# Kernel tuning notes

Measured on AMD Instinct MI355X. Metric: run time of the kernel, lower is better.

The kernel has to match this reference:

```python
import jax, jax.numpy as jnp
import numpy as np

NC = 6          # num_classes
RM = 16         # reg_max
TOPK = 10       # tal_topk
IMG = 640.0
STRIDES = (8, 16, 32)
BS = 32
NGT = 20        # GT boxes per image (uniform -> static max_boxes)


def _iou(b1, b2, ciou, eps=1e-7):
    x1 = jnp.maximum(b1[..., 0], b2[..., 0]); y1 = jnp.maximum(b1[..., 1], b2[..., 1])
    x2 = jnp.minimum(b1[..., 2], b2[..., 2]); y2 = jnp.minimum(b1[..., 3], b2[..., 3])
    inter = jnp.maximum(x2 - x1, 0.0) * jnp.maximum(y2 - y1, 0.0)
    w1 = jnp.maximum(b1[..., 2] - b1[..., 0], eps); h1 = jnp.maximum(b1[..., 3] - b1[..., 1], eps)
    w2 = jnp.maximum(b2[..., 2] - b2[..., 0], eps); h2 = jnp.maximum(b2[..., 3] - b2[..., 1], eps)
    union = w1 * h1 + w2 * h2 - inter + eps
    iou = inter / union
    if not ciou:
        return iou
    cw = jnp.maximum(b1[..., 2], b2[..., 2]) - jnp.minimum(b1[..., 0], b2[..., 0])
    ch = jnp.maximum(b1[..., 3], b2[..., 3]) - jnp.minimum(b1[..., 1], b2[..., 1])
    c2 = cw ** 2 + ch ** 2 + eps
    rho2 = ((b1[..., 0] + b1[..., 2] - b2[..., 0] - b2[..., 2]) ** 2
            + (b1[..., 1] + b1[..., 3] - b2[..., 1] - b2[..., 3]) ** 2) / 4.0
    v = (4.0 / (np.pi ** 2)) * (jnp.arctan(w2 / h2) - jnp.arctan(w1 / h1)) ** 2
    alpha = jax.lax.stop_gradient(v / (v - iou + (1.0 + eps)))
    return iou - (rho2 / c2 + v * alpha)


def _forward(p0, p1, p2, targets):
    bs = p0.shape[0]
    regs, clss, ancs, strs = [], [], [], []
    for p, s in zip((p0, p1, p2), STRIDES):
        b, c, h, w = p.shape
        p = jnp.transpose(p, (0, 2, 3, 1)).reshape(b, h * w, c)
        regs.append(p[..., :4 * RM].reshape(b, h * w, 4, RM))
        clss.append(p[..., 4 * RM:])
        gy, gx = jnp.meshgrid(jnp.arange(h), jnp.arange(w), indexing='ij')
        ancs.append(((jnp.stack([gx, gy], -1).astype(jnp.float32) + 0.5) * s).reshape(-1, 2))
        strs.append(jnp.full((h * w, 1), float(s), jnp.float32))
    pred_reg = jnp.concatenate(regs, 1)      # [bs, A, 4, RM]
    pred_cls = jnp.concatenate(clss, 1)      # [bs, A, NC]
    anchors = jnp.concatenate(ancs, 0)       # [A, 2] pixel coords
    stride_a = jnp.concatenate(strs, 0)      # [A, 1]
    A = anchors.shape[0]

    proj = jnp.arange(RM, dtype=jnp.float32)
    pd_dist = jnp.sum(jax.nn.softmax(pred_reg, -1) * proj, -1)       # [bs, A, 4]
    anc_b = jnp.broadcast_to(anchors[None], (bs, A, 2))
    pd_boxes = jnp.concatenate([anc_b - pd_dist[..., :2] * stride_a,
                                anc_b + pd_dist[..., 2:] * stride_a], -1)

    # GT parse: exactly NGT rows per image, grouped by image index (static reshape)
    G = targets.shape[0] // bs
    t = targets.reshape(bs, G, 6)
    gt_labels = t[..., 1]
    xywh = t[..., 2:6] * IMG
    gt_boxes = jnp.concatenate([xywh[..., :2] - xywh[..., 2:] / 2,
                                xywh[..., :2] + xywh[..., 2:] / 2], -1)  # [bs, G, 4]
    mask_gt = jnp.ones((bs, G, 1), jnp.float32)

    # ---- task-aligned assignment (on detached preds) ----
    pscore = jax.nn.sigmoid(jax.lax.stop_gradient(pred_cls))
    pbox_d = jax.lax.stop_gradient(pd_boxes)
    ious = _iou(gt_boxes[:, :, None, :], pbox_d[:, None, :, :], False)   # [bs, G, A]
    labels_i = gt_labels.astype(jnp.int32)
    scores = jnp.einsum('bac,bgc->bga', pscore, jax.nn.one_hot(labels_i, NC, dtype=pscore.dtype))
    align = (scores ** 0.5) * (ious ** 6.0)
    lt = anc_b[:, None, :, :] - gt_boxes[:, :, None, :2]
    rb = gt_boxes[:, :, None, 2:] - anc_b[:, None, :, :]
    in_gts = jnp.min(jnp.concatenate([lt, rb], -1), -1) > 1e-9
    align = align * in_gts * mask_gt
    _, tk_idx = jax.lax.top_k(align, TOPK)
    bi = jnp.arange(bs)[:, None, None]; gi = jnp.arange(G)[None, :, None]
    mask_pos = jnp.zeros((bs, G, A), bool).at[bi, gi, tk_idx].set(True)
    mask_pos = mask_pos & (align > 0)
    multi = jnp.sum(mask_pos, 1) > 1                                   # [bs, A]
    full = jnp.moveaxis(jax.nn.one_hot(jnp.argmax(align, 1), G), -1, 1) > 0.5
    mask_pos = jnp.where(multi[:, None, :], full, mask_pos)

    fg = jnp.any(mask_pos, 1)                                          # [bs, A]
    gt_idx = jnp.argmax(mask_pos, 1)                                   # [bs, A] (first True)
    tb = jnp.take_along_axis(gt_boxes, jnp.broadcast_to(gt_idx[..., None], (bs, A, 4)), axis=1)
    target_boxes = jnp.where(fg[..., None], tb, 0.0)
    t_lab = jnp.take_along_axis(labels_i, gt_idx, axis=1)
    iou_fg = jnp.maximum(jax.lax.stop_gradient(_iou(pd_boxes, target_boxes, False)), 0.0)
    norm_align = align / (jnp.max(align, -1, keepdims=True) + 1e-9)
    norm_g = jnp.take_along_axis(norm_align, gt_idx[:, None, :], axis=1)[:, 0, :]
    sval = jnp.where(fg, norm_g * iou_fg, 0.0)
    target_scores = sval[..., None] * jax.nn.one_hot(t_lab, NC, dtype=jnp.float32)

    # cls: BCE with logits, sum / num_anchors
    x = pred_cls
    bce = jnp.maximum(x, 0.0) - x * target_scores + jnp.log1p(jnp.exp(-jnp.abs(x)))
    loss_cls = jnp.sum(bce) / float(A)

    fgf = fg.astype(jnp.float32)
    num_pos = jnp.maximum(jnp.sum(fgf), 1.0)

    # bbox: 1 - CIoU over positives
    ciou = _iou(pd_boxes, target_boxes, True)
    loss_bbox = jnp.sum((1.0 - ciou) * fgf) / num_pos

    # DFL
    ltrb = jnp.concatenate([(anc_b - target_boxes[..., :2]) / stride_a,
                            (target_boxes[..., 2:] - anc_b) / stride_a], -1)
    ltrb = jnp.clip(ltrb, 0.0, RM - 1.01)
    tl = ltrb.astype(jnp.int32)
    wl = (tl + 1).astype(jnp.float32) - ltrb
    wr = ltrb - tl.astype(jnp.float32)
    logZ = jax.nn.logsumexp(pred_reg, -1)                              # [bs, A, 4]
    ce_l = logZ - jnp.take_along_axis(pred_reg, tl[..., None], -1)[..., 0]
    ce_r = logZ - jnp.take_along_axis(pred_reg, (tl + 1)[..., None], -1)[..., 0]
    loss_dfl = jnp.sum(jnp.sum(ce_l * wl + ce_r * wr, -1) * fgf) / num_pos

    l_cls = loss_cls * 1.0
    l_bbox = loss_bbox * 7.5
    l_dfl = loss_dfl * 1.5
    return jnp.stack([l_cls + l_bbox + l_dfl, l_cls, l_bbox, jnp.asarray(0.0, jnp.float32), l_dfl])


def setup_inputs() -> dict:
    key = jax.random.key(0)
    k0, k1, k2, k3, k4, k5 = jax.random.split(key, 6)
    C = 4 * RM + NC
    p0 = jax.random.normal(k0, (BS, C, 80, 80), jnp.float32)
    p1 = jax.random.normal(k1, (BS, C, 40, 40), jnp.float32)
    p2 = jax.random.normal(k2, (BS, C, 20, 20), jnp.float32)
    bidx = jnp.repeat(jnp.arange(BS), NGT).astype(jnp.float32)
    lab = jax.random.randint(k3, (BS * NGT,), 0, NC).astype(jnp.float32)
    cxcy = jax.random.uniform(k4, (BS * NGT, 2), minval=0.2, maxval=0.8)
    wh = jax.random.uniform(k5, (BS * NGT, 2), minval=0.05, maxval=0.3)
    targets = jnp.concatenate([bidx[:, None], lab[:, None], cxcy, wh], 1)
    return {"p0": p0, "p1": p1, "p2": p2, "targets": targets}


def reference(p0, p1, p2, targets):
    return _forward(p0, p1, p2, targets)
```

## Files before the change

kernel.cpp:

```cpp
#include <hip/hip_runtime.h>
#include <math.h>

#define NC 6
#define RM 16
#define TOPK 10
#define BSZ 32
#define G 20
#define A_TOT 8400
#define NBA (BSZ * A_TOT)
#define NBLK_LOSS ((NBA + 255) / 256)
#define MAXCAND 1024

__device__ __forceinline__ void anchor_decode(int a, int& lvl, int& ai, int& w, int& hw, float& s) {
    if (a < 6400)      { lvl = 0; ai = a;        w = 80; hw = 6400; s = 8.f; }
    else if (a < 8000) { lvl = 1; ai = a - 6400; w = 40; hw = 1600; s = 16.f; }
    else               { lvl = 2; ai = a - 8000; w = 20; hw = 400;  s = 32.f; }
}

__global__ __launch_bounds__(256) void k_prep(
        const float* __restrict__ p0, const float* __restrict__ p1, const float* __restrict__ p2,
        float* __restrict__ pd_boxes, float* __restrict__ logZ, float* __restrict__ pcls) {
    int idx = blockIdx.x * 256 + threadIdx.x;
    if (idx >= NBA) return;
    int b = idx / A_TOT, a = idx % A_TOT;
    int lvl, ai, w, hw; float s;
    anchor_decode(a, lvl, ai, w, hw, s);
    const float* p = (lvl == 0) ? p0 : ((lvl == 1) ? p1 : p2);
    const float* base = p + (size_t)b * 70 * hw + ai;
    float ax = ((ai % w) + 0.5f) * s;
    float ay = ((ai / w) + 0.5f) * s;

    float dist[4], lz[4];
    for (int sd = 0; sd < 4; ++sd) {
        float v[RM];
        float m = -1e30f;
        #pragma unroll
        for (int k = 0; k < RM; ++k) {
            v[k] = base[(size_t)(sd * RM + k) * hw];
            m = fmaxf(m, v[k]);
        }
        float se = 0.f, sk = 0.f;
        #pragma unroll
        for (int k = 0; k < RM; ++k) {
            float e = expf(v[k] - m);
            se += e;
            sk += e * (float)k;
        }
        dist[sd] = sk / se;
        lz[sd] = m + logf(se);
    }
    float4 box;
    box.x = ax - dist[0] * s;
    box.y = ay - dist[1] * s;
    box.z = ax + dist[2] * s;
    box.w = ay + dist[3] * s;
    ((float4*)pd_boxes)[idx] = box;
    ((float4*)logZ)[idx] = make_float4(lz[0], lz[1], lz[2], lz[3]);
    #pragma unroll
    for (int c = 0; c < NC; ++c)
        pcls[(size_t)c * NBA + idx] = base[(size_t)(64 + c) * hw];
}

__device__ __forceinline__ bool cand_better(float av, int ai_, float bv, int bi_) {
    if (av > bv) return true;
    if (av < bv) return false;
    if (ai_ < 0) return false;
    if (bi_ < 0) return true;
    return ai_ < bi_;
}

__global__ __launch_bounds__(256) void k_align(
        const float* __restrict__ targets,
        const float* __restrict__ pd_boxes, const float* __restrict__ pcls,
        float* __restrict__ align, float* __restrict__ amax, unsigned int* __restrict__ mask) {
    __shared__ float cval[MAXCAND];
    __shared__ int   cidx[MAXCAND];
    __shared__ int   cnt_s;
    __shared__ float rv[4];
    __shared__ int   ri[4];
    __shared__ float win_v_s;
    __shared__ int   win_i_s;

    int bg = blockIdx.x;
    int b = bg / G;
    int g = bg % G;
    const float* t = targets + (size_t)bg * 6;
    float cx = t[2] * 640.f, cy = t[3] * 640.f;
    float hw_ = t[4] * 320.f, hh = t[5] * 320.f;
    float gx1 = cx - hw_, gy1 = cy - hh, gx2 = cx + hw_, gy2 = cy + hh;
    int lab = (int)t[1];
    const float* pc = pcls + (size_t)lab * NBA + (size_t)b * A_TOT;
    const float4* pb = (const float4*)pd_boxes + (size_t)b * A_TOT;
    float* arow = align + (size_t)bg * A_TOT;
    const float eps = 1e-7f;
    float gw = fmaxf(gx2 - gx1, eps), gh = fmaxf(gy2 - gy1, eps);
    float garea = gw * gh;

    if (threadIdx.x == 0) cnt_s = 0;
    __syncthreads();

    for (int a = threadIdx.x; a < A_TOT; a += 256) {
        float4 box = pb[a];
        float x1 = fmaxf(gx1, box.x), y1 = fmaxf(gy1, box.y);
        float x2 = fminf(gx2, box.z), y2 = fminf(gy2, box.w);
        float inter = fmaxf(x2 - x1, 0.f) * fmaxf(y2 - y1, 0.f);
        float w2 = fmaxf(box.z - box.x, eps), h2 = fmaxf(box.w - box.y, eps);
        float uni = garea + w2 * h2 - inter + eps;
        float iou = inter / uni;
        float sc = 1.f / (1.f + expf(-pc[a]));
        int lvl, ai, w_, hwc; float s;
        anchor_decode(a, lvl, ai, w_, hwc, s);
        float ax = ((ai % w_) + 0.5f) * s, ay = ((ai / w_) + 0.5f) * s;
        float mn = fminf(fminf(ax - gx1, ay - gy1), fminf(gx2 - ax, gy2 - ay));
        float al = 0.f;
        if (mn > 1e-9f) {
            float i2 = iou * iou;
            al = sqrtf(sc) * (i2 * i2 * i2);
        }
        arow[a] = al;
        if (al > 0.f) {
            int p = atomicAdd(&cnt_s, 1);
            if (p < MAXCAND) { cval[p] = al; cidx[p] = a; }
        }
    }
    __syncthreads();
    int cnt = min(cnt_s, MAXCAND);

    float mv[MAXCAND / 256];
    int   mi[MAXCAND / 256];
    #pragma unroll
    for (int r = 0; r < MAXCAND / 256; ++r) {
        int p = threadIdx.x + r * 256;
        mv[r] = (p < cnt) ? cval[p] : -1.f;
        mi[r] = (p < cnt) ? cidx[p] : -1;
    }

    int lane = threadIdx.x & 63, wv = threadIdx.x >> 6;
    for (int it = 0; it < TOPK; ++it) {
        float v = -1.f; int vi = -1;
        #pragma unroll
        for (int r = 0; r < MAXCAND / 256; ++r)
            if (cand_better(mv[r], mi[r], v, vi)) { v = mv[r]; vi = mi[r]; }
        #pragma unroll
        for (int off = 32; off > 0; off >>= 1) {
            float ov = __shfl_down(v, off);
            int   oi = __shfl_down(vi, off);
            if (cand_better(ov, oi, v, vi)) { v = ov; vi = oi; }
        }
        if (lane == 0) { rv[wv] = v; ri[wv] = vi; }
        __syncthreads();
        if (threadIdx.x == 0) {
            float v0 = rv[0]; int i0 = ri[0];
            for (int i = 1; i < 4; ++i)
                if (cand_better(rv[i], ri[i], v0, i0)) { v0 = rv[i]; i0 = ri[i]; }
            if (it == 0) amax[bg] = fmaxf(v0, 0.f);
            if (i0 >= 0 && v0 > 0.f) atomicOr(&mask[(size_t)b * A_TOT + i0], 1u << g);
            win_v_s = v0; win_i_s = i0;
        }
        __syncthreads();
        int wi = win_i_s;
        if (wi < 0) break;
        #pragma unroll
        for (int r = 0; r < MAXCAND / 256; ++r)
            if (mi[r] == wi) { mv[r] = -1.f; mi[r] = -1; }
    }
}

__global__ __launch_bounds__(256) void k_loss(
        const float* __restrict__ targets,
        const float* __restrict__ pd_boxes, const float* __restrict__ logZ,
        const float* __restrict__ pcls, const float* __restrict__ align,
        const float* __restrict__ amax, const unsigned int* __restrict__ mask,
        const float* __restrict__ p0, const float* __restrict__ p1, const float* __restrict__ p2,
        float* __restrict__ partial) {
    int idx = blockIdx.x * 256 + threadIdx.x;
    float bce_s = 0.f, bbox_s = 0.f, dfl_s = 0.f, fg_s = 0.f;
    if (idx < NBA) {
        int b = idx / A_TOT, a = idx % A_TOT;
        unsigned int m = mask[idx];
        if (__popc(m) > 1) {
            float best = -1.f; int bg_ = 0;
            for (int g = 0; g < G; ++g) {
                float x = align[((size_t)b * G + g) * A_TOT + a];
                if (x > best) { best = x; bg_ = g; }
            }
            m = 1u << bg_;
        }
        bool fg = (m != 0u);
        float4 box = ((const float4*)pd_boxes)[idx];
        float tbx1 = 0.f, tby1 = 0.f, tbx2 = 0.f, tby2 = 0.f;
        float sval = 0.f; int lab = -1;
        const float eps = 1e-7f;
        if (fg) {
            int gidx = __ffs(m) - 1;
            const float* t = targets + ((size_t)b * G + gidx) * 6;
            lab = (int)t[1];
            float cx = t[2] * 640.f, cy = t[3] * 640.f;
            float hw_ = t[4] * 320.f, hh = t[5] * 320.f;
            tbx1 = cx - hw_; tby1 = cy - hh; tbx2 = cx + hw_; tby2 = cy + hh;
            float x1 = fmaxf(box.x, tbx1), y1 = fmaxf(box.y, tby1);
            float x2 = fminf(box.z, tbx2), y2 = fminf(box.w, tby2);
            float inter = fmaxf(x2 - x1, 0.f) * fmaxf(y2 - y1, 0.f);
            float w1 = fmaxf(box.z - box.x, eps), h1 = fmaxf(box.w - box.y, eps);
            float w2 = fmaxf(tbx2 - tbx1, eps), h2 = fmaxf(tby2 - tby1, eps);
            float uni = w1 * h1 + w2 * h2 - inter + eps;
            float iou_fg = fmaxf(inter / uni, 0.f);
            float al = align[((size_t)b * G + gidx) * A_TOT + a];
            sval = (al / (amax[b * G + gidx] + 1e-9f)) * iou_fg;
            fg_s = 1.f;
        }
        #pragma unroll
        for (int c = 0; c < NC; ++c) {
            float x = pcls[(size_t)c * NBA + idx];
            float ts = (fg && c == lab) ? sval : 0.f;
            bce_s += fmaxf(x, 0.f) - x * ts + log1pf(expf(-fabsf(x)));
        }
        if (fg) {
            float x1 = fmaxf(box.x, tbx1), y1 = fmaxf(box.y, tby1);
            float x2 = fminf(box.z, tbx2), y2 = fminf(box.w, tby2);
            float inter = fmaxf(x2 - x1, 0.f) * fmaxf(y2 - y1, 0.f);
            float w1 = fmaxf(box.z - box.x, eps), h1 = fmaxf(box.w - box.y, eps);
            float w2 = fmaxf(tbx2 - tbx1, eps), h2 = fmaxf(tby2 - tby1, eps);
            float uni = w1 * h1 + w2 * h2 - inter + eps;
            float iou = inter / uni;
            float cw = fmaxf(box.z, tbx2) - fminf(box.x, tbx1);
            float ch = fmaxf(box.w, tby2) - fminf(box.y, tby1);
            float c2 = cw * cw + ch * ch + eps;
            float dx = box.x + box.z - tbx1 - tbx2;
            float dy = box.y + box.w - tby1 - tby2;
            float rho2 = (dx * dx + dy * dy) * 0.25f;
            float dv = atanf(w2 / h2) - atanf(w1 / h1);
            float v = 0.40528473f * dv * dv;
            float alpha = v / (v - iou + (1.f + eps));
            float ciou = iou - (rho2 / c2 + v * alpha);
            bbox_s = 1.f - ciou;
            int lvl, ai, w_, hwc; float s;
            anchor_decode(a, lvl, ai, w_, hwc, s);
            float ax = ((ai % w_) + 0.5f) * s, ay = ((ai / w_) + 0.5f) * s;
            const float* p = (lvl == 0) ? p0 : ((lvl == 1) ? p1 : p2);
            const float* base = p + (size_t)b * 70 * hwc + ai;
            float4 lzv = ((const float4*)logZ)[idx];
            float lz[4] = {lzv.x, lzv.y, lzv.z, lzv.w};
            float lt[4] = {(ax - tbx1) / s, (ay - tby1) / s, (tbx2 - ax) / s, (tby2 - ay) / s};
            #pragma unroll
            for (int sd = 0; sd < 4; ++sd) {
                float d = fminf(fmaxf(lt[sd], 0.f), (float)RM - 1.01f);
                int tl = (int)d;
                float wl = (float)(tl + 1) - d;
                float wr = d - (float)tl;
                float xl = base[(size_t)(sd * RM + tl) * hwc];
                float xr = base[(size_t)(sd * RM + tl + 1) * hwc];
                dfl_s += (lz[sd] - xl) * wl + (lz[sd] - xr) * wr;
            }
        }
    }
    __shared__ float part[4][4];
    int lane = threadIdx.x & 63, wv = threadIdx.x >> 6;
    #pragma unroll
    for (int off = 32; off > 0; off >>= 1) {
        bce_s  += __shfl_down(bce_s,  off);
        bbox_s += __shfl_down(bbox_s, off);
        dfl_s  += __shfl_down(dfl_s,  off);
        fg_s   += __shfl_down(fg_s,   off);
    }
    if (lane == 0) {
        part[wv][0] = bce_s; part[wv][1] = bbox_s;
        part[wv][2] = dfl_s; part[wv][3] = fg_s;
    }
    __syncthreads();
    if (threadIdx.x == 0) {
        float s0 = 0.f, s1 = 0.f, s2 = 0.f, s3 = 0.f;
        for (int i = 0; i < 4; ++i) {
            s0 += part[i][0]; s1 += part[i][1]; s2 += part[i][2]; s3 += part[i][3];
        }
        float4* pp = (float4*)partial;
        pp[blockIdx.x] = make_float4(s0, s1, s2, s3);
    }
}

__global__ __launch_bounds__(256) void k_final(const float* __restrict__ partial,
                                               float* __restrict__ out) {
    double s0 = 0., s1 = 0., s2 = 0., s3 = 0.;
    for (int i = threadIdx.x; i < NBLK_LOSS; i += 256) {
        float4 p = ((const float4*)partial)[i];
        s0 += p.x; s1 += p.y; s2 += p.z; s3 += p.w;
    }
    #pragma unroll
    for (int off = 32; off > 0; off >>= 1) {
        s0 += __shfl_down(s0, off);
        s1 += __shfl_down(s1, off);
        s2 += __shfl_down(s2, off);
        s3 += __shfl_down(s3, off);
    }
    __shared__ double part[4][4];
    int lane = threadIdx.x & 63, wv = threadIdx.x >> 6;
    if (lane == 0) { part[wv][0] = s0; part[wv][1] = s1; part[wv][2] = s2; part[wv][3] = s3; }
    __syncthreads();
    if (threadIdx.x == 0) {
        double bce = 0., bbox = 0., dfl = 0., fgc = 0.;
        for (int i = 0; i < 4; ++i) {
            bce += part[i][0]; bbox += part[i][1]; dfl += part[i][2]; fgc += part[i][3];
        }
        double l_cls = bce / (double)A_TOT;
        double np_ = fmax(fgc, 1.0);
        double l_bbox = 7.5 * bbox / np_;
        double l_dfl = 1.5 * dfl / np_;
        out[0] = (float)(l_cls + l_bbox + l_dfl);
        out[1] = (float)l_cls;
        out[2] = (float)l_bbox;
        out[3] = 0.f;
        out[4] = (float)l_dfl;
    }
}

extern "C" void kernel_launch(void* const* d_in, const int* in_sizes, int n_in,
                              void* d_out, int out_size, void* d_ws, size_t ws_size,
                              hipStream_t stream) {
    const float* p0 = (const float*)d_in[0];
    const float* p1 = (const float*)d_in[1];
    const float* p2 = (const float*)d_in[2];
    const float* targets = (const float*)d_in[3];
    float* out = (float*)d_out;

    char* ws = (char*)d_ws;
    size_t off = 0;
    float* pd_boxes = (float*)(ws + off); off += (size_t)NBA * 4 * sizeof(float);
    float* logZ     = (float*)(ws + off); off += (size_t)NBA * 4 * sizeof(float);
    float* pcls     = (float*)(ws + off); off += (size_t)NC * NBA * sizeof(float);
    float* align    = (float*)(ws + off); off += (size_t)BSZ * G * A_TOT * sizeof(float);
    float* amax     = (float*)(ws + off); off += (size_t)BSZ * G * sizeof(float);
    unsigned int* mask = (unsigned int*)(ws + off); off += (size_t)NBA * sizeof(unsigned int);
    float* partial  = (float*)(ws + off); off += (size_t)NBLK_LOSS * 4 * sizeof(float);

    hipMemsetAsync(mask, 0, (size_t)NBA * sizeof(unsigned int), stream);

    k_prep<<<(NBA + 255) / 256, 256, 0, stream>>>(p0, p1, p2, pd_boxes, logZ, pcls);
    k_align<<<BSZ * G, 256, 0, stream>>>(targets, pd_boxes, pcls, align, amax, mask);
    k_loss<<<NBLK_LOSS, 256, 0, stream>>>(targets, pd_boxes, logZ, pcls, align,
                                          amax, mask, p0, p1, p2, partial);
    k_final<<<1, 256, 0, stream>>>(partial, out);
}
```

Baseline: 151.6 us.

## Vectorize prep, recompute align scores instead of storing them, split BCE

```diff
diff --git a/kernel.cpp b/kernel.cpp
--- a/kernel.cpp
+++ b/kernel.cpp
@@ -9,7 +9,10 @@
 #define A_TOT 8400
 #define NBA (BSZ * A_TOT)
 #define NBLK_LOSS ((NBA + 255) / 256)
+#define NBLK_PREP ((NBA / 4 + 255) / 256)
 #define MAXCAND 1024
+
+#define COMP(v4, j) ((j) == 0 ? (v4).x : (j) == 1 ? (v4).y : (j) == 2 ? (v4).z : (v4).w)
 
 __device__ __forceinline__ void anchor_decode(int a, int& lvl, int& ai, int& w, int& hw, float& s) {
     if (a < 6400)      { lvl = 0; ai = a;        w = 80; hw = 6400; s = 8.f; }
@@ -17,48 +20,97 @@
     else               { lvl = 2; ai = a - 8000; w = 20; hw = 400;  s = 32.f; }
 }
 
+__device__ __forceinline__ float align_from(const float* __restrict__ trow, float logit,
+                                            float4 box, float ax, float ay) {
+    float cx = trow[2] * 640.f, cy = trow[3] * 640.f;
+    float hwd = trow[4] * 320.f, hh = trow[5] * 320.f;
+    float gx1 = cx - hwd, gy1 = cy - hh, gx2 = cx + hwd, gy2 = cy + hh;
+    float mn = fminf(fminf(ax - gx1, ay - gy1), fminf(gx2 - ax, gy2 - ay));
+    if (mn <= 1e-9f) return 0.f;
+    const float eps = 1e-7f;
+    float x1 = fmaxf(gx1, box.x), y1 = fmaxf(gy1, box.y);
+    float x2 = fminf(gx2, box.z), y2 = fminf(gy2, box.w);
+    float inter = fmaxf(x2 - x1, 0.f) * fmaxf(y2 - y1, 0.f);
+    float gw = fmaxf(gx2 - gx1, eps), gh = fmaxf(gy2 - gy1, eps);
+    float w2 = fmaxf(box.z - box.x, eps), h2 = fmaxf(box.w - box.y, eps);
+    float uni = gw * gh + w2 * h2 - inter + eps;
+    float iou = inter / uni;
+    float sc = 1.f / (1.f + __expf(-logit));
+    float i2 = iou * iou;
+    return sqrtf(sc) * (i2 * i2 * i2);
+}
+
 __global__ __launch_bounds__(256) void k_prep(
         const float* __restrict__ p0, const float* __restrict__ p1, const float* __restrict__ p2,
-        float* __restrict__ pd_boxes, float* __restrict__ logZ, float* __restrict__ pcls) {
-    int idx = blockIdx.x * 256 + threadIdx.x;
-    if (idx >= NBA) return;
-    int b = idx / A_TOT, a = idx % A_TOT;
-    int lvl, ai, w, hw; float s;
-    anchor_decode(a, lvl, ai, w, hw, s);
-    const float* p = (lvl == 0) ? p0 : ((lvl == 1) ? p1 : p2);
-    const float* base = p + (size_t)b * 70 * hw + ai;
-    float ax = ((ai % w) + 0.5f) * s;
-    float ay = ((ai / w) + 0.5f) * s;
-
-    float dist[4], lz[4];
-    for (int sd = 0; sd < 4; ++sd) {
-        float v[RM];
-        float m = -1e30f;
-        #pragma unroll
-        for (int k = 0; k < RM; ++k) {
-            v[k] = base[(size_t)(sd * RM + k) * hw];
-            m = fmaxf(m, v[k]);
-        }
-        float se = 0.f, sk = 0.f;
-        #pragma unroll
-        for (int k = 0; k < RM; ++k) {
-            float e = expf(v[k] - m);
-            se += e;
-            sk += e * (float)k;
-        }
-        dist[sd] = sk / se;
-        lz[sd] = m + logf(se);
-    }
-    float4 box;
-    box.x = ax - dist[0] * s;
-    box.y = ay - dist[1] * s;
-    box.z = ax + dist[2] * s;
-    box.w = ay + dist[3] * s;
-    ((float4*)pd_boxes)[idx] = box;
-    ((float4*)logZ)[idx] = make_float4(lz[0], lz[1], lz[2], lz[3]);
+        float* __restrict__ pd_boxes, float* __restrict__ logZ,
+        unsigned int* __restrict__ mask, float* __restrict__ partial_prep) {
+    int tid = blockIdx.x * 256 + threadIdx.x;
+    int idx4 = tid * 4;
+    float bce = 0.f;
+    if (idx4 < NBA) {
+        int b = idx4 / A_TOT, a4 = idx4 % A_TOT;
+        int lvl, ai, w, hw; float s;
+        anchor_decode(a4, lvl, ai, w, hw, s);
+        const float* p = (lvl == 0) ? p0 : ((lvl == 1) ? p1 : p2);
+        const float* base = p + (size_t)b * 70 * hw + ai;
+        float ay = ((float)(ai / w) + 0.5f) * s;
+        float ax0 = ((float)(ai % w) + 0.5f) * s;
+
+        float4 dist0, dist1, dist2, dist3, lz0, lz1, lz2, lz3;
+        auto do_side = [&](int sd, float4& dist, float4& lz) {
+            float4 v[RM];
+            float4 m = make_float4(-1e30f, -1e30f, -1e30f, -1e30f);
+            #pragma unroll
+            for (int k = 0; k < RM; ++k) {
+                v[k] = *(const float4*)(base + (size_t)(sd * RM + k) * hw);
+                m.x = fmaxf(m.x, v[k].x); m.y = fmaxf(m.y, v[k].y);
+                m.z = fmaxf(m.z, v[k].z); m.w = fmaxf(m.w, v[k].w);
+            }
+            float4 se = make_float4(0, 0, 0, 0), sk = make_float4(0, 0, 0, 0);
+            #pragma unroll
+            for (int k = 0; k < RM; ++k) {
+                float fk = (float)k;
+                float ex = __expf(v[k].x - m.x); se.x += ex; sk.x += ex * fk;
+                float ey = __expf(v[k].y - m.y); se.y += ey; sk.y += ey * fk;
+                float ez = __expf(v[k].z - m.z); se.z += ez; sk.z += ez * fk;
+                float ew = __expf(v[k].w - m.w); se.w += ew; sk.w += ew * fk;
+            }
+            dist = make_float4(sk.x / se.x, sk.y / se.y, sk.z / se.z, sk.w / se.w);
+            lz = make_float4(m.x + __logf(se.x), m.y + __logf(se.y),
+                             m.z + __logf(se.z), m.w + __logf(se.w));
+        };
+        do_side(0, dist0, lz0);
+        do_side(1, dist1, lz1);
+        do_side(2, dist2, lz2);
+        do_side(3, dist3, lz3);
+
+        #pragma unroll
+        for (int j = 0; j < 4; ++j) {
+            float axj = ax0 + (float)j * s;
+            float4 bx = make_float4(axj - COMP(dist0, j) * s, ay - COMP(dist1, j) * s,
+                                    axj + COMP(dist2, j) * s, ay + COMP(dist3, j) * s);
+            ((float4*)pd_boxes)[idx4 + j] = bx;
+            ((float4*)logZ)[idx4 + j] =
+                make_float4(COMP(lz0, j), COMP(lz1, j), COMP(lz2, j), COMP(lz3, j));
+        }
+        #pragma unroll
+        for (int c = 0; c < NC; ++c) {
+            float4 x = *(const float4*)(base + (size_t)(64 + c) * hw);
+            bce += fmaxf(x.x, 0.f) + __logf(1.f + __expf(-fabsf(x.x)));
+            bce += fmaxf(x.y, 0.f) + __logf(1.f + __expf(-fabsf(x.y)));
+            bce += fmaxf(x.z, 0.f) + __logf(1.f + __expf(-fabsf(x.z)));
+            bce += fmaxf(x.w, 0.f) + __logf(1.f + __expf(-fabsf(x.w)));
+        }
+        ((uint4*)mask)[tid] = make_uint4(0, 0, 0, 0);
+    }
+    __shared__ float part[4];
+    int lane = threadIdx.x & 63, wv = threadIdx.x >> 6;
     #pragma unroll
-    for (int c = 0; c < NC; ++c)
-        pcls[(size_t)c * NBA + idx] = base[(size_t)(64 + c) * hw];
+    for (int off = 32; off > 0; off >>= 1) bce += __shfl_down(bce, off);
+    if (lane == 0) part[wv] = bce;
+    __syncthreads();
+    if (threadIdx.x == 0)
+        partial_prep[blockIdx.x] = part[0] + part[1] + part[2] + part[3];
 }
 
 __device__ __forceinline__ bool cand_better(float av, int ai_, float bv, int bi_) {
@@ -71,53 +123,35 @@
 
 __global__ __launch_bounds__(256) void k_align(
         const float* __restrict__ targets,
-        const float* __restrict__ pd_boxes, const float* __restrict__ pcls,
-        float* __restrict__ align, float* __restrict__ amax, unsigned int* __restrict__ mask) {
+        const float* __restrict__ pd_boxes,
+        const float* __restrict__ p0, const float* __restrict__ p1, const float* __restrict__ p2,
+        float* __restrict__ amax, unsigned int* __restrict__ mask) {
     __shared__ float cval[MAXCAND];
     __shared__ int   cidx[MAXCAND];
     __shared__ int   cnt_s;
     __shared__ float rv[4];
     __shared__ int   ri[4];
-    __shared__ float win_v_s;
     __shared__ int   win_i_s;
 
     int bg = blockIdx.x;
     int b = bg / G;
     int g = bg % G;
     const float* t = targets + (size_t)bg * 6;
-    float cx = t[2] * 640.f, cy = t[3] * 640.f;
-    float hw_ = t[4] * 320.f, hh = t[5] * 320.f;
-    float gx1 = cx - hw_, gy1 = cy - hh, gx2 = cx + hw_, gy2 = cy + hh;
     int lab = (int)t[1];
-    const float* pc = pcls + (size_t)lab * NBA + (size_t)b * A_TOT;
+    const float* cb0 = p0 + (size_t)b * 70 * 6400 + (size_t)(64 + lab) * 6400;
+    const float* cb1 = p1 + (size_t)b * 70 * 1600 + (size_t)(64 + lab) * 1600;
+    const float* cb2 = p2 + (size_t)b * 70 * 400  + (size_t)(64 + lab) * 400;
     const float4* pb = (const float4*)pd_boxes + (size_t)b * A_TOT;
-    float* arow = align + (size_t)bg * A_TOT;
-    const float eps = 1e-7f;
-    float gw = fmaxf(gx2 - gx1, eps), gh = fmaxf(gy2 - gy1, eps);
-    float garea = gw * gh;
 
     if (threadIdx.x == 0) cnt_s = 0;
     __syncthreads();
 
     for (int a = threadIdx.x; a < A_TOT; a += 256) {
-        float4 box = pb[a];
-        float x1 = fmaxf(gx1, box.x), y1 = fmaxf(gy1, box.y);
-        float x2 = fminf(gx2, box.z), y2 = fminf(gy2, box.w);
-        float inter = fmaxf(x2 - x1, 0.f) * fmaxf(y2 - y1, 0.f);
-        float w2 = fmaxf(box.z - box.x, eps), h2 = fmaxf(box.w - box.y, eps);
-        float uni = garea + w2 * h2 - inter + eps;
-        float iou = inter / uni;
-        float sc = 1.f / (1.f + expf(-pc[a]));
         int lvl, ai, w_, hwc; float s;
         anchor_decode(a, lvl, ai, w_, hwc, s);
         float ax = ((ai % w_) + 0.5f) * s, ay = ((ai / w_) + 0.5f) * s;
-        float mn = fminf(fminf(ax - gx1, ay - gy1), fminf(gx2 - ax, gy2 - ay));
-        float al = 0.f;
-        if (mn > 1e-9f) {
-            float i2 = iou * iou;
-            al = sqrtf(sc) * (i2 * i2 * i2);
-        }
-        arow[a] = al;
+        float logit = (lvl == 0) ? cb0[ai] : ((lvl == 1) ? cb1[ai] : cb2[ai]);
+        float al = align_from(t, logit, pb[a], ax, ay);
         if (al > 0.f) {
             int p = atomicAdd(&cnt_s, 1);
             if (p < MAXCAND) { cval[p] = al; cidx[p] = a; }
@@ -155,7 +189,7 @@
                 if (cand_better(rv[i], ri[i], v0, i0)) { v0 = rv[i]; i0 = ri[i]; }
             if (it == 0) amax[bg] = fmaxf(v0, 0.f);
             if (i0 >= 0 && v0 > 0.f) atomicOr(&mask[(size_t)b * A_TOT + i0], 1u << g);
-            win_v_s = v0; win_i_s = i0;
+            win_i_s = i0;
         }
         __syncthreads();
         int wi = win_i_s;
@@ -169,53 +203,41 @@
 __global__ __launch_bounds__(256) void k_loss(
         const float* __restrict__ targets,
         const float* __restrict__ pd_boxes, const float* __restrict__ logZ,
-        const float* __restrict__ pcls, const float* __restrict__ align,
         const float* __restrict__ amax, const unsigned int* __restrict__ mask,
         const float* __restrict__ p0, const float* __restrict__ p1, const float* __restrict__ p2,
         float* __restrict__ partial) {
     int idx = blockIdx.x * 256 + threadIdx.x;
     float bce_s = 0.f, bbox_s = 0.f, dfl_s = 0.f, fg_s = 0.f;
     if (idx < NBA) {
-        int b = idx / A_TOT, a = idx % A_TOT;
         unsigned int m = mask[idx];
-        if (__popc(m) > 1) {
-            float best = -1.f; int bg_ = 0;
-            for (int g = 0; g < G; ++g) {
-                float x = align[((size_t)b * G + g) * A_TOT + a];
-                if (x > best) { best = x; bg_ = g; }
+        if (m != 0u) {
+            int b = idx / A_TOT, a = idx % A_TOT;
+            int lvl, ai, w_, hw; float s;
+            anchor_decode(a, lvl, ai, w_, hw, s);
+            const float* p = (lvl == 0) ? p0 : ((lvl == 1) ? p1 : p2);
+            const float* base = p + (size_t)b * 70 * hw + ai;
+            float ax = ((ai % w_) + 0.5f) * s, ay = ((ai / w_) + 0.5f) * s;
+            float4 box = ((const float4*)pd_boxes)[idx];
+            int gidx;
+            if (__popc(m) > 1) {
+                float best = -1.f; gidx = 0;
+                for (int g = 0; g < G; ++g) {
+                    const float* tg = targets + ((size_t)b * G + g) * 6;
+                    int labg = (int)tg[1];
+                    float al = align_from(tg, base[(size_t)(64 + labg) * hw], box, ax, ay);
+                    if (al > best) { best = al; gidx = g; }
+                }
+            } else {
+                gidx = __ffs(m) - 1;
             }
-            m = 1u << bg_;
-        }
-        bool fg = (m != 0u);
-        float4 box = ((const float4*)pd_boxes)[idx];
-        float tbx1 = 0.f, tby1 = 0.f, tbx2 = 0.f, tby2 = 0.f;
-        float sval = 0.f; int lab = -1;
-        const float eps = 1e-7f;
-        if (fg) {
-            int gidx = __ffs(m) - 1;
             const float* t = targets + ((size_t)b * G + gidx) * 6;
-            lab = (int)t[1];
+            int lab = (int)t[1];
+            float logit = base[(size_t)(64 + lab) * hw];
+            float al = align_from(t, logit, box, ax, ay);
             float cx = t[2] * 640.f, cy = t[3] * 640.f;
-            float hw_ = t[4] * 320.f, hh = t[5] * 320.f;
-            tbx1 = cx - hw_; tby1 = cy - hh; tbx2 = cx + hw_; tby2 = cy + hh;
-            float x1 = fmaxf(box.x, tbx1), y1 = fmaxf(box.y, tby1);
-            float x2 = fminf(box.z, tbx2), y2 = fminf(box.w, tby2);
-            float inter = fmaxf(x2 - x1, 0.f) * fmaxf(y2 - y1, 0.f);
-            float w1 = fmaxf(box.z - box.x, eps), h1 = fmaxf(box.w - box.y, eps);
-            float w2 = fmaxf(tbx2 - tbx1, eps), h2 = fmaxf(tby2 - tby1, eps);
-            float uni = w1 * h1 + w2 * h2 - inter + eps;
-            float iou_fg = fmaxf(inter / uni, 0.f);
-            float al = align[((size_t)b * G + gidx) * A_TOT + a];
-            sval = (al / (amax[b * G + gidx] + 1e-9f)) * iou_fg;
-            fg_s = 1.f;
-        }
-        #pragma unroll
-        for (int c = 0; c < NC; ++c) {
-            float x = pcls[(size_t)c * NBA + idx];
-            float ts = (fg && c == lab) ? sval : 0.f;
-            bce_s += fmaxf(x, 0.f) - x * ts + log1pf(expf(-fabsf(x)));
-        }
-        if (fg) {
+            float hwd = t[4] * 320.f, hh = t[5] * 320.f;
+            float tbx1 = cx - hwd, tby1 = cy - hh, tbx2 = cx + hwd, tby2 = cy + hh;
+            const float eps = 1e-7f;
             float x1 = fmaxf(box.x, tbx1), y1 = fmaxf(box.y, tby1);
             float x2 = fminf(box.z, tbx2), y2 = fminf(box.w, tby2);
             float inter = fmaxf(x2 - x1, 0.f) * fmaxf(y2 - y1, 0.f);
@@ -223,6 +245,10 @@
             float w2 = fmaxf(tbx2 - tbx1, eps), h2 = fmaxf(tby2 - tby1, eps);
             float uni = w1 * h1 + w2 * h2 - inter + eps;
             float iou = inter / uni;
+            float iou_fg = fmaxf(iou, 0.f);
+            float sval = (al / (amax[b * G + gidx] + 1e-9f)) * iou_fg;
+            bce_s = -logit * sval;
+            fg_s = 1.f;
             float cw = fmaxf(box.z, tbx2) - fminf(box.x, tbx1);
             float ch = fmaxf(box.w, tby2) - fminf(box.y, tby1);
             float c2 = cw * cw + ch * ch + eps;
@@ -234,11 +260,6 @@
             float alpha = v / (v - iou + (1.f + eps));
             float ciou = iou - (rho2 / c2 + v * alpha);
             bbox_s = 1.f - ciou;
-            int lvl, ai, w_, hwc; float s;
-            anchor_decode(a, lvl, ai, w_, hwc, s);
-            float ax = ((ai % w_) + 0.5f) * s, ay = ((ai / w_) + 0.5f) * s;
-            const float* p = (lvl == 0) ? p0 : ((lvl == 1) ? p1 : p2);
-            const float* base = p + (size_t)b * 70 * hwc + ai;
             float4 lzv = ((const float4*)logZ)[idx];
             float lz[4] = {lzv.x, lzv.y, lzv.z, lzv.w};
             float lt[4] = {(ax - tbx1) / s, (ay - tby1) / s, (tbx2 - ax) / s, (tby2 - ay) / s};
@@ -248,8 +269,8 @@
                 int tl = (int)d;
                 float wl = (float)(tl + 1) - d;
                 float wr = d - (float)tl;
-                float xl = base[(size_t)(sd * RM + tl) * hwc];
-                float xr = base[(size_t)(sd * RM + tl + 1) * hwc];
+                float xl = base[(size_t)(sd * RM + tl) * hw];
+                float xr = base[(size_t)(sd * RM + tl + 1) * hw];
                 dfl_s += (lz[sd] - xl) * wl + (lz[sd] - xr) * wr;
             }
         }
@@ -273,18 +294,20 @@
         for (int i = 0; i < 4; ++i) {
             s0 += part[i][0]; s1 += part[i][1]; s2 += part[i][2]; s3 += part[i][3];
         }
-        float4* pp = (float4*)partial;
-        pp[blockIdx.x] = make_float4(s0, s1, s2, s3);
+        ((float4*)partial)[blockIdx.x] = make_float4(s0, s1, s2, s3);
     }
 }
 
 __global__ __launch_bounds__(256) void k_final(const float* __restrict__ partial,
+                                               const float* __restrict__ partial_prep,
                                                float* __restrict__ out) {
     double s0 = 0., s1 = 0., s2 = 0., s3 = 0.;
     for (int i = threadIdx.x; i < NBLK_LOSS; i += 256) {
         float4 p = ((const float4*)partial)[i];
         s0 += p.x; s1 += p.y; s2 += p.z; s3 += p.w;
     }
+    for (int i = threadIdx.x; i < NBLK_PREP; i += 256)
+        s0 += partial_prep[i];
     #pragma unroll
     for (int off = 32; off > 0; off >>= 1) {
         s0 += __shfl_down(s0, off);
@@ -326,17 +349,14 @@
     size_t off = 0;
     float* pd_boxes = (float*)(ws + off); off += (size_t)NBA * 4 * sizeof(float);
     float* logZ     = (float*)(ws + off); off += (size_t)NBA * 4 * sizeof(float);
-    float* pcls     = (float*)(ws + off); off += (size_t)NC * NBA * sizeof(float);
-    float* align    = (float*)(ws + off); off += (size_t)BSZ * G * A_TOT * sizeof(float);
     float* amax     = (float*)(ws + off); off += (size_t)BSZ * G * sizeof(float);
     unsigned int* mask = (unsigned int*)(ws + off); off += (size_t)NBA * sizeof(unsigned int);
     float* partial  = (float*)(ws + off); off += (size_t)NBLK_LOSS * 4 * sizeof(float);
-
-    hipMemsetAsync(mask, 0, (size_t)NBA * sizeof(unsigned int), stream);
-
-    k_prep<<<(NBA + 255) / 256, 256, 0, stream>>>(p0, p1, p2, pd_boxes, logZ, pcls);
-    k_align<<<BSZ * G, 256, 0, stream>>>(targets, pd_boxes, pcls, align, amax, mask);
-    k_loss<<<NBLK_LOSS, 256, 0, stream>>>(targets, pd_boxes, logZ, pcls, align,
-                                          amax, mask, p0, p1, p2, partial);
-    k_final<<<1, 256, 0, stream>>>(partial, out);
-}
+    float* partial_prep = (float*)(ws + off); off += (size_t)NBLK_PREP * sizeof(float);
+
+    k_prep<<<NBLK_PREP, 256, 0, stream>>>(p0, p1, p2, pd_boxes, logZ, mask, partial_prep);
+    k_align<<<BSZ * G, 256, 0, stream>>>(targets, pd_boxes, p0, p1, p2, amax, mask);
+    k_loss<<<NBLK_LOSS, 256, 0, stream>>>(targets, pd_boxes, logZ, amax, mask,
+                                          p0, p1, p2, partial);
+    k_final<<<1, 256, 0, stream>>>(partial, partial_prep, out);
+}
```

Result: slower. 157.8 us (+4.1%).
